# Kernel optimization log

Hardware: AMD Instinct MI355X
Metric: run time of the kernel (lower is better)

Reference implementation:

```python
import jax, jax.numpy as jnp
import numpy as np

B, D, K, M1, M2 = 256, 128, 32, 64, 32   # batch, n_nodes, K copies, dims[1], dims[2]
H1, H2, L = 128, 64, 32                   # pivae_dims


def setup_inputs() -> dict:
    key = jax.random.key(0)
    ks = iter(jax.random.split(key, 32))

    def rn(shape, scale):
        return jax.random.normal(next(ks), shape, dtype=jnp.float32) * scale

    x = jax.random.normal(next(ks), (B, D), dtype=jnp.float32)

    # per-node fc1 weights: [D, M1, D]; bounds force nonneg with zero diag column
    W1_pos = jnp.abs(rn((D, M1, D), 1.0 / np.sqrt(D)))
    W1_neg = jnp.abs(rn((D, M1, D), 1.0 / np.sqrt(D)))
    eye = jnp.eye(D, dtype=jnp.float32)[:, None, :]   # zero out W[j,:,j]
    W1_pos = W1_pos * (1.0 - eye)
    W1_neg = W1_neg * (1.0 - eye)
    b1_pos = rn((D, M1), 0.02)
    b1_neg = rn((D, M1), 0.02)

    # LocallyConnected stacks: weight [K, m_in, m_out]
    lc1_w = rn((K, M1, M2), 1.0 / np.sqrt(M1)); lc1_b = rn((K, M2), 0.02)
    lc2_w = rn((K, M2, 1), 1.0 / np.sqrt(M2));  lc2_b = rn((K, 1), 0.02)

    # per-sample beta Linear(k,1): weights [B, K], bias [B]
    beta_w = rn((B, K), 1.0 / np.sqrt(K)); beta_b = rn((B,), 0.02)

    # VAE params (encoder -> mu/logvar -> decoder), stored as (in,out) matrices
    enc1_w = rn((K, H1), 1.0 / np.sqrt(K));  enc1_b = jnp.zeros((H1,), jnp.float32)
    enc2_w = rn((H1, H2), 1.0 / np.sqrt(H1)); enc2_b = jnp.zeros((H2,), jnp.float32)
    mu_w = rn((H2, L), 1.0 / np.sqrt(H2));    mu_b = jnp.zeros((L,), jnp.float32)
    lv_w = rn((H2, L), 1.0 / np.sqrt(H2));    lv_b = jnp.zeros((L,), jnp.float32)
    dec1_w = rn((L, H2), 1.0 / np.sqrt(L));   dec1_b = jnp.zeros((H2,), jnp.float32)
    dec2_w = rn((H2, H1), 1.0 / np.sqrt(H2)); dec2_b = jnp.zeros((H1,), jnp.float32)
    dec3_w = rn((H1, K), 1.0 / np.sqrt(H1));  dec3_b = jnp.zeros((K,), jnp.float32)

    eps = jax.random.normal(next(ks), (B, L), dtype=jnp.float32)  # reparam noise

    return dict(x=x, W1_pos=W1_pos, W1_neg=W1_neg, b1_pos=b1_pos, b1_neg=b1_neg,
                lc1_w=lc1_w, lc1_b=lc1_b, lc2_w=lc2_w, lc2_b=lc2_b,
                beta_w=beta_w, beta_b=beta_b,
                enc1_w=enc1_w, enc1_b=enc1_b, enc2_w=enc2_w, enc2_b=enc2_b,
                mu_w=mu_w, mu_b=mu_b, lv_w=lv_w, lv_b=lv_b,
                dec1_w=dec1_w, dec1_b=dec1_b, dec2_w=dec2_w, dec2_b=dec2_b,
                dec3_w=dec3_w, dec3_b=dec3_b, eps=eps)


def reference(x, W1_pos, W1_neg, b1_pos, b1_neg, lc1_w, lc1_b, lc2_w, lc2_b,
              beta_w, beta_b, enc1_w, enc1_b, enc2_w, enc2_b, mu_w, mu_b,
              lv_w, lv_b, dec1_w, dec1_b, dec2_w, dec2_b, dec3_w, dec3_b, eps):
    b, d = x.shape
    k = lc1_w.shape[0]

    # fused per-node fc1: (pos - neg) applied to x with column j zeroed, all j at once
    W1 = W1_pos - W1_neg                      # [D, M1, D]
    b1 = b1_pos - b1_neg                      # [D, M1]
    full = jnp.einsum('bi,jhi->bjh', x, W1)   # as if no column were zeroed
    diagW = jnp.einsum('jhj->jh', W1)         # [D, M1] column-j weight of node j
    phi = full - x[:, :, None] * diagW[None] + b1[None]   # [B, D, M1]

    # expand to K copies, run sigmoid + LocallyConnected stack
    h = jnp.broadcast_to(phi[:, :, None, :], (b, d, k, phi.shape[-1]))
    h = jnp.einsum('bdkm,kmn->bdkn', jax.nn.sigmoid(h), lc1_w) + lc1_b   # [B,D,K,M2]
    h = jnp.einsum('bdkm,kmn->bdkn', jax.nn.sigmoid(h), lc2_w) + lc2_b   # [B,D,K,1]
    last_phi_x = h[..., 0]                    # [B, D, K]

    # per-sample beta projection (batched over B)
    y1 = jnp.einsum('bdk,bk->bd', last_phi_x, beta_w) + beta_b[:, None]

    # VAE on the stacked beta weights [B, K]
    e = jax.nn.relu(beta_w @ enc1_w + enc1_b)
    e = jax.nn.relu(e @ enc2_w + enc2_b)
    mu = e @ mu_w + mu_b
    logvar = e @ lv_w + lv_b
    z = mu + eps * jnp.exp(0.5 * logvar)
    dh = jax.nn.relu(z @ dec1_w + dec1_b)
    dh = jax.nn.relu(dh @ dec2_w + dec2_b)
    recon = dh @ dec3_w + dec3_b              # [B, K]

    y2 = jnp.einsum('bdk,bk->bd', last_phi_x, recon) + beta_b[:, None]
    return (y1, y2, mu, logvar)
```

## Files before the change

kernel.cpp:

```cpp
#include <hip/hip_runtime.h>
#include <stdint.h>

#define BB 256
#define DD 128
#define KK 32
#define MM1 64
#define MM2 32

typedef __attribute__((ext_vector_type(8))) short bf16x8;
typedef __attribute__((ext_vector_type(4))) float f32x4;

#define LOG2E 1.44269504088896f


__device__ __forceinline__ short f2b(float f) {
  uint32_t u = __builtin_bit_cast(uint32_t, f);
  u += 0x7FFFu + ((u >> 16) & 1u);
  return (short)(u >> 16);
}
__device__ __forceinline__ float sigm_pre(float acc, float cpre) {
  return __builtin_amdgcn_rcpf(
      1.0f + __builtin_amdgcn_exp2f(fmaf(acc, -LOG2E, cpre)));
}

__global__ __launch_bounds__(256) void combo_kernel(
    const float* __restrict__ x, const float* __restrict__ W1p,
    const float* __restrict__ W1n, const float* __restrict__ b1p,
    const float* __restrict__ b1n, const float* __restrict__ lc1w,
    const float* __restrict__ lc1b, const float* __restrict__ lc2b,
    const float* __restrict__ betaw,
    const float* __restrict__ enc1w, const float* __restrict__ enc1b,
    const float* __restrict__ enc2w, const float* __restrict__ enc2b,
    const float* __restrict__ muw,  const float* __restrict__ mub,
    const float* __restrict__ lvw,  const float* __restrict__ lvb,
    const float* __restrict__ dec1w, const float* __restrict__ dec1b,
    const float* __restrict__ dec2w, const float* __restrict__ dec2b,
    const float* __restrict__ dec3w, const float* __restrict__ dec3b,
    const float* __restrict__ eps,
    char* __restrict__ ws, float* __restrict__ mu_out,
    float* __restrict__ lv_out)
{
  const int bx = blockIdx.x;
  if (bx < 1024) {
    const int tid = bx * 256 + threadIdx.x;
    {
      float4 a = ((const float4*)W1p)[tid];
      float4 b = ((const float4*)W1n)[tid];
      short4 s;
      s.x = f2b(a.x - b.x); s.y = f2b(a.y - b.y);
      s.z = f2b(a.z - b.z); s.w = f2b(a.w - b.w);
      ((short4*)(ws + 303104))[tid] = s;
    }
    if (tid < 8192) {
      float4 v = ((const float4*)x)[tid];
      short4 s;
      s.x = f2b(v.x); s.y = f2b(v.y); s.z = f2b(v.z); s.w = f2b(v.w);
      ((short4*)(ws + 65536))[tid] = s;
    }
    if (tid < 65536) {
      int k = tid >> 11, n = (tid >> 6) & 31, m = tid & 63;
      ((short*)(ws + 131072))[tid] = f2b(lc1w[k * 2048 + m * 32 + n]);
    }
    if (tid < 8192) {
      ((float*)(ws + 32768))[tid] = betaw[(tid & 255) * 32 + (tid >> 8)];
    }
    if (tid < 1024) { ((float*)(ws + 262144))[tid] = -lc1b[tid] * LOG2E; }
    if (tid < 32) { ((float*)(ws + 266240))[tid] = 0.25f * lc2b[tid]; }
    if (tid < 8192) {
      ((float*)(ws + 270336))[tid] = -(b1p[tid] - b1n[tid]) * LOG2E;
    }
    return;
  }

  const int b = bx - 1024, t = threadIdx.x;
  float* reconT = (float*)ws;
  __shared__ float bw[KK], e1[128], e2[64], zz[32], d1s[64], d2s[128];
  if (t < KK) bw[t] = betaw[b * KK + t];
  __syncthreads();
  if (t < 128) {
    float a0 = enc1b[t], a1 = 0.f;
    #pragma unroll
    for (int k = 0; k < KK; k += 2) {
      a0 = fmaf(bw[k], enc1w[k * 128 + t], a0);
      a1 = fmaf(bw[k + 1], enc1w[(k + 1) * 128 + t], a1);
    }
    e1[t] = fmaxf(a0 + a1, 0.f);
  }
  __syncthreads();
  if (t < 64) {
    float a0 = enc2b[t], a1 = 0.f, a2 = 0.f, a3 = 0.f;
    #pragma unroll 8
    for (int h = 0; h < 128; h += 4) {
      a0 = fmaf(e1[h], enc2w[h * 64 + t], a0);
      a1 = fmaf(e1[h + 1], enc2w[(h + 1) * 64 + t], a1);
      a2 = fmaf(e1[h + 2], enc2w[(h + 2) * 64 + t], a2);
      a3 = fmaf(e1[h + 3], enc2w[(h + 3) * 64 + t], a3);
    }
    e2[t] = fmaxf((a0 + a1) + (a2 + a3), 0.f);
  }
  __syncthreads();
  if (t < 32) {
    float m0 = mub[t], m1 = 0.f, l0 = lvb[t], l1 = 0.f;
    #pragma unroll 8
    for (int h = 0; h < 64; h += 2) {
      float ea = e2[h], eb = e2[h + 1];
      m0 = fmaf(ea, muw[h * 32 + t], m0);
      m1 = fmaf(eb, muw[(h + 1) * 32 + t], m1);
      l0 = fmaf(ea, lvw[h * 32 + t], l0);
      l1 = fmaf(eb, lvw[(h + 1) * 32 + t], l1);
    }
    float m = m0 + m1, l = l0 + l1;
    mu_out[b * 32 + t] = m;
    lv_out[b * 32 + t] = l;
    zz[t] = fmaf(eps[b * 32 + t], __expf(0.5f * l), m);
  }
  __syncthreads();
  if (t < 64) {
    float a0 = dec1b[t], a1 = 0.f;
    #pragma unroll
    for (int l = 0; l < 32; l += 2) {
      a0 = fmaf(zz[l], dec1w[l * 64 + t], a0);
      a1 = fmaf(zz[l + 1], dec1w[(l + 1) * 64 + t], a1);
    }
    d1s[t] = fmaxf(a0 + a1, 0.f);
  }
  __syncthreads();
  if (t < 128) {
    float a0 = dec2b[t], a1 = 0.f, a2 = 0.f, a3 = 0.f;
    #pragma unroll 8
    for (int h = 0; h < 64; h += 4) {
      a0 = fmaf(d1s[h], dec2w[h * 128 + t], a0);
      a1 = fmaf(d1s[h + 1], dec2w[(h + 1) * 128 + t], a1);
      a2 = fmaf(d1s[h + 2], dec2w[(h + 2) * 128 + t], a2);
      a3 = fmaf(d1s[h + 3], dec2w[(h + 3) * 128 + t], a3);
    }
    d2s[t] = fmaxf((a0 + a1) + (a2 + a3), 0.f);
  }
  __syncthreads();
  if (t < 32) {
    float a0 = dec3b[t], a1 = 0.f, a2 = 0.f, a3 = 0.f;
    #pragma unroll 8
    for (int h = 0; h < 128; h += 4) {
      a0 = fmaf(d2s[h], dec3w[h * 32 + t], a0);
      a1 = fmaf(d2s[h + 1], dec3w[(h + 1) * 32 + t], a1);
      a2 = fmaf(d2s[h + 2], dec3w[(h + 2) * 32 + t], a2);
      a3 = fmaf(d2s[h + 3], dec3w[(h + 3) * 32 + t], a3);
    }
    reconT[t * BB + b] = (a0 + a1) + (a2 + a3);
  }
}

__global__ __launch_bounds__(512) void main_kernel(
    const float* __restrict__ lc2w, const float* __restrict__ betab,
    const char* __restrict__ ws, float* __restrict__ out)
{
  const int bx = blockIdx.x;
  const int d = bx >> 2;
  const int bq = bx & 3;
  const int tid = threadIdx.x;
  const int wv = tid >> 6, lane = tid & 63;
  const int g = lane >> 4, l15 = lane & 15;

  const short* __restrict__ xbf   = (const short*)(ws + 65536);
  const short* __restrict__ lc1T  = (const short*)(ws + 131072);
  const float* __restrict__ lc1bs = (const float*)(ws + 262144);
  const float* __restrict__ lc2bq = (const float*)(ws + 266240);
  const float* __restrict__ b1s   = (const float*)(ws + 270336);
  const short* __restrict__ w1bf  = (const short*)(ws + 303104);
  const float* __restrict__ betaT = (const float*)(ws + 32768);
  const float* __restrict__ recT  = (const float*)(ws + 0);

  __shared__ __align__(16) short sS[64 * 64];
  __shared__ __align__(16) float betaS[KK * 64];
  __shared__ __align__(16) float reconS[KK * 64];
  __shared__ __align__(16) float cS[KK * MM2];
  __shared__ __align__(16) float wSS[KK * MM2];
  __shared__ float lbq[KK];
  __shared__ float yred[8][64][2];

  {
    const int k = tid >> 4, j = (tid & 15) * 4;
    *(float4*)&betaS[k * 64 + j]  = *(const float4*)&betaT[k * BB + bq * 64 + j];
    *(float4*)&reconS[k * 64 + j] = *(const float4*)&recT[k * BB + bq * 64 + j];
  }
  if (tid < 256)      ((f32x4*)cS)[tid]        = ((const f32x4*)lc1bs)[tid];
  else if (tid < 512) ((f32x4*)wSS)[tid - 256] = ((const f32x4*)lc2w)[tid - 256];
  if (tid < KK) lbq[tid] = lc2bq[tid];

  {
    const int bt = wv >> 1, mtp = (wv & 1) * 2;
    const short* xrow = xbf + (bq * 64 + bt * 16 + l15) * DD + g * 8;
    bf16x8 xa[4];
    #pragma unroll
    for (int ks = 0; ks < 4; ++ks)
      xa[ks] = *(const bf16x8*)(xrow + ks * 32);
    const short* wrow = w1bf + d * (MM1 * DD);
    #pragma unroll
    for (int mi = 0; mi < 2; ++mi) {
      const int m = (mtp + mi) * 16 + l15;
      f32x4 acc = {0.f, 0.f, 0.f, 0.f};
      #pragma unroll
      for (int ks = 0; ks < 4; ++ks) {
        bf16x8 wb = *(const bf16x8*)(wrow + m * DD + ks * 32 + g * 8);
        acc = __builtin_amdgcn_mfma_f32_16x16x32_bf16(xa[ks], wb, acc, 0, 0, 0);
      }
      const float cpre = b1s[d * MM1 + m];
      #pragma unroll
      for (int r = 0; r < 4; ++r) {
        const int bl = bt * 16 + g * 4 + r;
        sS[bl * 64 + ((m & ~7) ^ ((bl & 7) << 3)) + (m & 7)] =
            f2b(sigm_pre(acc[r], cpre));
      }
    }
  }
  __syncthreads();

  float y1p[4] = {0, 0, 0, 0}, y2p[4] = {0, 0, 0, 0};

  #pragma unroll
  for (int kk = 0; kk < 4; ++kk) {
    const int k = wv * 4 + kk;
    const short* ap = lc1T + (k * 32 + l15) * 64 + g * 8;
    const bf16x8 A00 = *(const bf16x8*)(ap);
    const bf16x8 A01 = *(const bf16x8*)(ap + 32);
    const bf16x8 A10 = *(const bf16x8*)(ap + 16 * 64);
    const bf16x8 A11 = *(const bf16x8*)(ap + 16 * 64 + 32);
    const f32x4 c40 = *(const f32x4*)&cS[k * 32 + g * 4];
    const f32x4 c41 = *(const f32x4*)&cS[k * 32 + 16 + g * 4];
    const f32x4 w40 = *(const f32x4*)&wSS[k * 32 + g * 4];
    const f32x4 w41 = *(const f32x4*)&wSS[k * 32 + 16 + g * 4];
    const float lb = lbq[k];

    #pragma unroll
    for (int rt = 0; rt < 4; ++rt) {
      const int b = rt * 16 + l15;
      const int bsw = (b & 7) << 3;
      const bf16x8 sa0 = *(const bf16x8*)&sS[b * 64 + ((g * 8) ^ bsw)];
      const bf16x8 sa1 = *(const bf16x8*)&sS[b * 64 + ((32 + g * 8) ^ bsw)];
      f32x4 a0 = {0.f, 0.f, 0.f, 0.f}, a1 = {0.f, 0.f, 0.f, 0.f};
      a0 = __builtin_amdgcn_mfma_f32_16x16x32_bf16(A00, sa0, a0, 0, 0, 0);
      a0 = __builtin_amdgcn_mfma_f32_16x16x32_bf16(A01, sa1, a0, 0, 0, 0);
      a1 = __builtin_amdgcn_mfma_f32_16x16x32_bf16(A10, sa0, a1, 0, 0, 0);
      a1 = __builtin_amdgcn_mfma_f32_16x16x32_bf16(A11, sa1, a1, 0, 0, 0);
      float v = lb;
      #pragma unroll
      for (int r = 0; r < 4; ++r) {
        v = fmaf(sigm_pre(a0[r], c40[r]), w40[r], v);
        v = fmaf(sigm_pre(a1[r], c41[r]), w41[r], v);
      }
      y1p[rt] = fmaf(v, betaS[k * 64 + rt * 16 + l15], y1p[rt]);
      y2p[rt] = fmaf(v, reconS[k * 64 + rt * 16 + l15], y2p[rt]);
    }
  }

  #pragma unroll
  for (int rt = 0; rt < 4; ++rt) {
    y1p[rt] += __shfl_xor(y1p[rt], 16, 64);
    y1p[rt] += __shfl_xor(y1p[rt], 32, 64);
    y2p[rt] += __shfl_xor(y2p[rt], 16, 64);
    y2p[rt] += __shfl_xor(y2p[rt], 32, 64);
  }
  if (g == 0) {
    #pragma unroll
    for (int rt = 0; rt < 4; ++rt) {
      yred[wv][rt * 16 + l15][0] = y1p[rt];
      yred[wv][rt * 16 + l15][1] = y2p[rt];
    }
  }
  __syncthreads();
  if (tid < 128) {
    const int bl = tid >> 1, o = tid & 1;
    float s = 0.f;
    #pragma unroll
    for (int w = 0; w < 8; ++w) s += yred[w][bl][o];
    const int b = bq * 64 + bl;
    out[o * (BB * DD) + b * DD + d] = s + betab[b];
  }
}

extern "C" void kernel_launch(void* const* d_in, const int* in_sizes, int n_in,
                              void* d_out, int out_size, void* d_ws, size_t ws_size,
                              hipStream_t stream) {
  const float* x     = (const float*)d_in[0];
  const float* W1p   = (const float*)d_in[1];
  const float* W1n   = (const float*)d_in[2];
  const float* b1p   = (const float*)d_in[3];
  const float* b1n   = (const float*)d_in[4];
  const float* lc1w  = (const float*)d_in[5];
  const float* lc1b  = (const float*)d_in[6];
  const float* lc2w  = (const float*)d_in[7];
  const float* lc2b  = (const float*)d_in[8];
  const float* betaw = (const float*)d_in[9];
  const float* betab = (const float*)d_in[10];
  const float* enc1w = (const float*)d_in[11];
  const float* enc1b = (const float*)d_in[12];
  const float* enc2w = (const float*)d_in[13];
  const float* enc2b = (const float*)d_in[14];
  const float* muw   = (const float*)d_in[15];
  const float* mub   = (const float*)d_in[16];
  const float* lvw   = (const float*)d_in[17];
  const float* lvb   = (const float*)d_in[18];
  const float* dec1w = (const float*)d_in[19];
  const float* dec1b = (const float*)d_in[20];
  const float* dec2w = (const float*)d_in[21];
  const float* dec2b = (const float*)d_in[22];
  const float* dec3w = (const float*)d_in[23];
  const float* dec3b = (const float*)d_in[24];
  const float* eps   = (const float*)d_in[25];

  float* out    = (float*)d_out;
  char*  ws     = (char*)d_ws;
  float* mu_out = out + BB * DD * 2;
  float* lv_out = mu_out + BB * 32;

  combo_kernel<<<dim3(1280), dim3(256), 0, stream>>>(
      x, W1p, W1n, b1p, b1n, lc1w, lc1b, lc2b, betaw,
      enc1w, enc1b, enc2w, enc2b, muw, mub, lvw, lvb,
      dec1w, dec1b, dec2w, dec2b, dec3w, dec3b, eps,
      ws, mu_out, lv_out);

  main_kernel<<<dim3(512), dim3(512), 0, stream>>>(
      lc2w, betab, (const char*)ws, out);
}
```

Baseline: 135.4 us.

## Process two nodes per block and overlap phase-1 GEMM with phase-2

Each main_kernel block now handles two nodes d instead of one, halving the grid to 256 blocks. The lc1 A-fragments are loaded once into registers and reused for both nodes, and the phase-1 sigmoid GEMM for the second node is issued before phase-2 of the first, using double-buffered shared memory. This amortizes per-block setup loads and lets the two phases overlap. In exchange it raises register and LDS pressure, and on a GPU with 256 CUs the smaller grid gives each CU only one block, so there is less parallelism to hide latency.

```diff
diff --git a/kernel.cpp b/kernel.cpp
--- a/kernel.cpp
+++ b/kernel.cpp
@@ -155,8 +155,9 @@
     const char* __restrict__ ws, float* __restrict__ out)
 {
   const int bx = blockIdx.x;
-  const int d = bx >> 2;
+  const int dp = bx >> 2;
   const int bq = bx & 3;
+  const int d0 = dp * 2, d1 = d0 + 1;
   const int tid = threadIdx.x;
   const int wv = tid >> 6, lane = tid & 63;
   const int g = lane >> 4, l15 = lane & 15;
@@ -170,13 +171,13 @@
   const float* __restrict__ betaT = (const float*)(ws + 32768);
   const float* __restrict__ recT  = (const float*)(ws + 0);
 
-  __shared__ __align__(16) short sS[64 * 64];
+  __shared__ __align__(16) short sS[2][64 * 64];
   __shared__ __align__(16) float betaS[KK * 64];
   __shared__ __align__(16) float reconS[KK * 64];
   __shared__ __align__(16) float cS[KK * MM2];
   __shared__ __align__(16) float wSS[KK * MM2];
   __shared__ float lbq[KK];
-  __shared__ float yred[8][64][2];
+  __shared__ float yred[8][64][4];
 
   {
     const int k = tid >> 4, j = (tid & 15) * 4;
@@ -187,94 +188,112 @@
   else if (tid < 512) ((f32x4*)wSS)[tid - 256] = ((const f32x4*)lc2w)[tid - 256];
   if (tid < KK) lbq[tid] = lc2bq[tid];
 
+  bf16x8 Af[4][2][2];
+  #pragma unroll
+  for (int kk = 0; kk < 4; ++kk) {
+    const short* ap = lc1T + ((wv * 4 + kk) * 32 + l15) * 64 + g * 8;
+    Af[kk][0][0] = *(const bf16x8*)(ap);
+    Af[kk][0][1] = *(const bf16x8*)(ap + 32);
+    Af[kk][1][0] = *(const bf16x8*)(ap + 16 * 64);
+    Af[kk][1][1] = *(const bf16x8*)(ap + 16 * 64 + 32);
+  }
+  const int bt = wv >> 1, mtp = (wv & 1) * 2;
+  bf16x8 xa[4];
   {
-    const int bt = wv >> 1, mtp = (wv & 1) * 2;
     const short* xrow = xbf + (bq * 64 + bt * 16 + l15) * DD + g * 8;
-    bf16x8 xa[4];
     #pragma unroll
     for (int ks = 0; ks < 4; ++ks)
       xa[ks] = *(const bf16x8*)(xrow + ks * 32);
-    const short* wrow = w1bf + d * (MM1 * DD);
-    #pragma unroll
-    for (int mi = 0; mi < 2; ++mi) {
-      const int m = (mtp + mi) * 16 + l15;
-      f32x4 acc = {0.f, 0.f, 0.f, 0.f};
-      #pragma unroll
-      for (int ks = 0; ks < 4; ++ks) {
-        bf16x8 wb = *(const bf16x8*)(wrow + m * DD + ks * 32 + g * 8);
-        acc = __builtin_amdgcn_mfma_f32_16x16x32_bf16(xa[ks], wb, acc, 0, 0, 0);
-      }
-      const float cpre = b1s[d * MM1 + m];
-      #pragma unroll
-      for (int r = 0; r < 4; ++r) {
-        const int bl = bt * 16 + g * 4 + r;
-        sS[bl * 64 + ((m & ~7) ^ ((bl & 7) << 3)) + (m & 7)] =
-            f2b(sigm_pre(acc[r], cpre));
-      }
-    }
-  }
-  __syncthreads();
-
-  float y1p[4] = {0, 0, 0, 0}, y2p[4] = {0, 0, 0, 0};
-
-  #pragma unroll
-  for (int kk = 0; kk < 4; ++kk) {
-    const int k = wv * 4 + kk;
-    const short* ap = lc1T + (k * 32 + l15) * 64 + g * 8;
-    const bf16x8 A00 = *(const bf16x8*)(ap);
-    const bf16x8 A01 = *(const bf16x8*)(ap + 32);
-    const bf16x8 A10 = *(const bf16x8*)(ap + 16 * 64);
-    const bf16x8 A11 = *(const bf16x8*)(ap + 16 * 64 + 32);
-    const f32x4 c40 = *(const f32x4*)&cS[k * 32 + g * 4];
-    const f32x4 c41 = *(const f32x4*)&cS[k * 32 + 16 + g * 4];
-    const f32x4 w40 = *(const f32x4*)&wSS[k * 32 + g * 4];
-    const f32x4 w41 = *(const f32x4*)&wSS[k * 32 + 16 + g * 4];
-    const float lb = lbq[k];
-
-    #pragma unroll
-    for (int rt = 0; rt < 4; ++rt) {
-      const int b = rt * 16 + l15;
-      const int bsw = (b & 7) << 3;
-      const bf16x8 sa0 = *(const bf16x8*)&sS[b * 64 + ((g * 8) ^ bsw)];
-      const bf16x8 sa1 = *(const bf16x8*)&sS[b * 64 + ((32 + g * 8) ^ bsw)];
-      f32x4 a0 = {0.f, 0.f, 0.f, 0.f}, a1 = {0.f, 0.f, 0.f, 0.f};
-      a0 = __builtin_amdgcn_mfma_f32_16x16x32_bf16(A00, sa0, a0, 0, 0, 0);
-      a0 = __builtin_amdgcn_mfma_f32_16x16x32_bf16(A01, sa1, a0, 0, 0, 0);
-      a1 = __builtin_amdgcn_mfma_f32_16x16x32_bf16(A10, sa0, a1, 0, 0, 0);
-      a1 = __builtin_amdgcn_mfma_f32_16x16x32_bf16(A11, sa1, a1, 0, 0, 0);
-      float v = lb;
-      #pragma unroll
-      for (int r = 0; r < 4; ++r) {
-        v = fmaf(sigm_pre(a0[r], c40[r]), w40[r], v);
-        v = fmaf(sigm_pre(a1[r], c41[r]), w41[r], v);
-      }
-      y1p[rt] = fmaf(v, betaS[k * 64 + rt * 16 + l15], y1p[rt]);
-      y2p[rt] = fmaf(v, reconS[k * 64 + rt * 16 + l15], y2p[rt]);
-    }
-  }
-
-  #pragma unroll
-  for (int rt = 0; rt < 4; ++rt) {
-    y1p[rt] += __shfl_xor(y1p[rt], 16, 64);
-    y1p[rt] += __shfl_xor(y1p[rt], 32, 64);
-    y2p[rt] += __shfl_xor(y2p[rt], 16, 64);
-    y2p[rt] += __shfl_xor(y2p[rt], 32, 64);
-  }
-  if (g == 0) {
-    #pragma unroll
-    for (int rt = 0; rt < 4; ++rt) {
-      yred[wv][rt * 16 + l15][0] = y1p[rt];
-      yred[wv][rt * 16 + l15][1] = y2p[rt];
-    }
-  }
-  __syncthreads();
-  if (tid < 128) {
-    const int bl = tid >> 1, o = tid & 1;
+  }
+
+#define PHASE1(dd, which) { \
+    const short* wrow = w1bf + (dd) * (MM1 * DD); \
+    _Pragma("unroll") \
+    for (int mi = 0; mi < 2; ++mi) { \
+      const int m = (mtp + mi) * 16 + l15; \
+      f32x4 acc = {0.f, 0.f, 0.f, 0.f}; \
+      _Pragma("unroll") \
+      for (int ks = 0; ks < 4; ++ks) { \
+        bf16x8 wb = *(const bf16x8*)(wrow + m * DD + ks * 32 + g * 8); \
+        acc = __builtin_amdgcn_mfma_f32_16x16x32_bf16(xa[ks], wb, acc, 0, 0, 0); \
+      } \
+      const float cpre = b1s[(dd) * MM1 + m]; \
+      _Pragma("unroll") \
+      for (int r = 0; r < 4; ++r) { \
+        const int bl = bt * 16 + g * 4 + r; \
+        sS[which][bl * 64 + ((m & ~7) ^ ((bl & 7) << 3)) + (m & 7)] = \
+            f2b(sigm_pre(acc[r], cpre)); \
+      } \
+    } }
+
+#define PHASE2(which, yoff) { \
+    bf16x8 sa[4][2]; \
+    _Pragma("unroll") \
+    for (int rt = 0; rt < 4; ++rt) { \
+      const int b = rt * 16 + l15; \
+      const int bsw = (b & 7) << 3; \
+      sa[rt][0] = *(const bf16x8*)&sS[which][b * 64 + ((g * 8) ^ bsw)]; \
+      sa[rt][1] = *(const bf16x8*)&sS[which][b * 64 + ((32 + g * 8) ^ bsw)]; \
+    } \
+    float y1p[4] = {0, 0, 0, 0}, y2p[4] = {0, 0, 0, 0}; \
+    _Pragma("unroll") \
+    for (int kk = 0; kk < 4; ++kk) { \
+      const int k = wv * 4 + kk; \
+      const f32x4 c40 = *(const f32x4*)&cS[k * 32 + g * 4]; \
+      const f32x4 c41 = *(const f32x4*)&cS[k * 32 + 16 + g * 4]; \
+      const f32x4 w40 = *(const f32x4*)&wSS[k * 32 + g * 4]; \
+      const f32x4 w41 = *(const f32x4*)&wSS[k * 32 + 16 + g * 4]; \
+      const float lb = lbq[k]; \
+      _Pragma("unroll") \
+      for (int rt = 0; rt < 4; ++rt) { \
+        f32x4 a0 = {0.f, 0.f, 0.f, 0.f}, a1 = {0.f, 0.f, 0.f, 0.f}; \
+        a0 = __builtin_amdgcn_mfma_f32_16x16x32_bf16(Af[kk][0][0], sa[rt][0], a0, 0, 0, 0); \
+        a0 = __builtin_amdgcn_mfma_f32_16x16x32_bf16(Af[kk][0][1], sa[rt][1], a0, 0, 0, 0); \
+        a1 = __builtin_amdgcn_mfma_f32_16x16x32_bf16(Af[kk][1][0], sa[rt][0], a1, 0, 0, 0); \
+        a1 = __builtin_amdgcn_mfma_f32_16x16x32_bf16(Af[kk][1][1], sa[rt][1], a1, 0, 0, 0); \
+        float v = lb; \
+        _Pragma("unroll") \
+        for (int r = 0; r < 4; ++r) { \
+          v = fmaf(sigm_pre(a0[r], c40[r]), w40[r], v); \
+          v = fmaf(sigm_pre(a1[r], c41[r]), w41[r], v); \
+        } \
+        y1p[rt] = fmaf(v, betaS[k * 64 + rt * 16 + l15], y1p[rt]); \
+        y2p[rt] = fmaf(v, reconS[k * 64 + rt * 16 + l15], y2p[rt]); \
+      } \
+    } \
+    _Pragma("unroll") \
+    for (int rt = 0; rt < 4; ++rt) { \
+      y1p[rt] += __shfl_xor(y1p[rt], 16, 64); \
+      y1p[rt] += __shfl_xor(y1p[rt], 32, 64); \
+      y2p[rt] += __shfl_xor(y2p[rt], 16, 64); \
+      y2p[rt] += __shfl_xor(y2p[rt], 32, 64); \
+    } \
+    if (g == 0) { \
+      _Pragma("unroll") \
+      for (int rt = 0; rt < 4; ++rt) { \
+        yred[wv][rt * 16 + l15][(yoff)]     = y1p[rt]; \
+        yred[wv][rt * 16 + l15][(yoff) + 1] = y2p[rt]; \
+      } \
+    } }
+
+  PHASE1(d0, 0);
+  __syncthreads();
+  PHASE1(d1, 1);
+  PHASE2(0, 0);
+  __syncthreads();
+  PHASE2(1, 2);
+  __syncthreads();
+
+#undef PHASE1
+#undef PHASE2
+
+  if (tid < 256) {
+    const int ds = tid >> 7, q = tid & 127, bl = q >> 1, o = q & 1;
     float s = 0.f;
     #pragma unroll
-    for (int w = 0; w < 8; ++w) s += yred[w][bl][o];
+    for (int w = 0; w < 8; ++w) s += yred[w][bl][ds * 2 + o];
     const int b = bq * 64 + bl;
-    out[o * (BB * DD) + b * DD + d] = s + betab[b];
+    out[o * (BB * DD) + b * DD + d0 + ds] = s + betab[b];
   }
 }
 
@@ -319,6 +338,6 @@
       dec1w, dec1b, dec2w, dec2b, dec3w, dec3b, eps,
       ws, mu_out, lv_out);
 
-  main_kernel<<<dim3(512), dim3(512), 0, stream>>>(
+  main_kernel<<<dim3(256), dim3(512), 0, stream>>>(
       lc2w, betab, (const char*)ws, out);
 }
```

After: 139.5 us. +3.1%, slower.
